# Kernel optimization log

Hardware: AMD Instinct MI355X
Metric: run time of the kernel (lower is better)

## Reference

```python
import jax, jax.numpy as jnp
import numpy as np

NUM_EMB = 1024
EMB_DIM = 256
COMM_COST = 0.25
BETA = 0.25


def setup_inputs() -> dict:
    key = jax.random.key(0)
    k1, k2 = jax.random.split(key)
    x = jax.random.normal(k1, (16, EMB_DIM, 64, 64), dtype=jnp.float32)
    # nn.Embedding initialized uniform(-1/num_emb, 1/num_emb)
    emb_weight = jax.random.uniform(
        k2, (NUM_EMB, EMB_DIM), dtype=jnp.float32,
        minval=-1.0 / NUM_EMB, maxval=1.0 / NUM_EMB)
    return {"x": x, "emb_weight": emb_weight}


def reference(x, emb_weight):
    # x: [B, C, H, W] -> [B, H, W, C]
    xp = jnp.transpose(x, (0, 2, 3, 1))
    B, H, W, C = xp.shape
    flat = xp.reshape(-1, C)  # [N, C]
    # squared euclidean distances (argmin-equivalent to torch.cdist)
    d2 = (jnp.sum(flat * flat, axis=1, keepdims=True)
          - 2.0 * jnp.einsum('nc,kc->nk', flat, emb_weight)
          + jnp.sum(emb_weight * emb_weight, axis=1))  # [N, K]
    idx = jnp.argmin(d2, axis=1)  # [N]
    quantized = emb_weight[idx].reshape(B, H, W, C)
    e_latent_loss = jnp.mean((jax.lax.stop_gradient(quantized) - xp) ** 2) * BETA
    q_latent_loss = jnp.mean((quantized - jax.lax.stop_gradient(xp)) ** 2)
    c_loss = q_latent_loss + COMM_COST * e_latent_loss
    # straight-through estimator
    quant_st = xp + jax.lax.stop_gradient(quantized - xp)
    quant_out = jnp.transpose(quant_st, (0, 3, 1, 2))  # [B, C, H, W]
    return (c_loss, quant_out)
```

## Files before the change

### kernel.cpp

```cpp
#include <hip/hip_runtime.h>
#include <hip/hip_bf16.h>
#include <cstdint>
#include <cstddef>

#define EMB_K   1024
#define EMB_C   256
#define HWB     4096
#define NPIX    65536

typedef __bf16 bf16x8 __attribute__((ext_vector_type(8)));
typedef float  f32x4  __attribute__((ext_vector_type(4)));

__device__ __forceinline__ unsigned short bf16bits(float v) {
  __hip_bfloat16 h = __float2bfloat16(v);
  return __builtin_bit_cast(unsigned short, h);
}

__global__ void k_emb(const float* __restrict__ emb, unsigned short* __restrict__ emb_bf,
                      float* __restrict__ enorm, float* __restrict__ loss) {
  int k = blockIdx.x;
  int c = threadIdx.x;
  if (k == 0 && c == 0) *loss = 0.f;
  float v = emb[(size_t)k * EMB_C + c];
  emb_bf[(size_t)k * EMB_C + c] = bf16bits(v);
  float s = v * v;
  for (int m = 32; m; m >>= 1) s += __shfl_down(s, m, 64);
  __shared__ float red[4];
  int lane = c & 63, w = c >> 6;
  if (lane == 0) red[w] = s;
  __syncthreads();
  if (c == 0) enorm[k] = red[0] + red[1] + red[2] + red[3];
}

__device__ __forceinline__ void stage64(const unsigned short* __restrict__ rows,
                                        unsigned char* buf, int t) {
#pragma unroll
  for (int j = 0; j < 4; ++j) {
    int d = j * 512 + t;
    int r = d >> 5;
    int slot = d & 31;
    int c16 = ((slot >> 3) << 3) | ((slot & 7) ^ (r & 7));
    const unsigned short* src = rows + (size_t)r * EMB_C + c16 * 8;
    __builtin_amdgcn_global_load_lds(
        (const __attribute__((address_space(1))) void*)src,
        (__attribute__((address_space(3))) void*)(buf + (unsigned)(j * 8192 + (t >> 6) * 1024)),
        16, 0, 0);
  }
}

__device__ __forceinline__ int posA(int cc, int nl) {
  return ((cc >> 3) << 3) | ((cc & 7) ^ ((nl ^ (nl >> 2)) & 7));
}

#define LDS_BYTES 137280

__global__ __launch_bounds__(512) void
k_main(const float* __restrict__ x, const unsigned short* __restrict__ embbf,
       const float* __restrict__ enorm, unsigned* __restrict__ keys_g,
       float* __restrict__ loss) {
  extern __shared__ char smem[];
  unsigned char* Abase = (unsigned char*)smem + 65536;
  float*    cjl    = (float*)(smem + 131072);
  unsigned* keys_l = (unsigned*)(smem + 135168);
  float*    xn_l   = (float*)(smem + 136192);
  float*    red    = (float*)(smem + 137216);

  int n0 = blockIdx.x * 256;
  int b  = n0 >> 12, hw0 = n0 & 4095;
  int t = threadIdx.x, w = t >> 6, lane = t & 63;
  int quad = lane >> 4, lr = lane & 15;
  int g  = w >> 1;
  int h2 = w & 1;

  stage64(embbf,               (unsigned char*)smem,         t);
  stage64(embbf + 64 * EMB_C,  (unsigned char*)smem + 32768, t);

  if (t < 256) { keys_l[t] = 0u; xn_l[t] = 0.f; }
  for (int i = t; i < 1024; i += 512) cjl[i] = 0.375f - 0.5f * enorm[i];
  __syncthreads();

  bf16x8 af[4][8];
#pragma unroll
  for (int p = 0; p < 2; ++p) {
    if (p) __syncthreads();
    {
      int hwq = t & 31;
      int cg  = t >> 5;
      const float* xp = x + (size_t)b * (EMB_C * HWB) + hw0 + p * 128 + hwq * 4;
      float xn[4] = {0.f, 0.f, 0.f, 0.f};
      unsigned pk[4][8] = {};
#pragma unroll
      for (int j = 0; j < 16; ++j) {
        f32x4 v = *(const f32x4*)(xp + (size_t)(cg * 16 + j) * HWB);
#pragma unroll
        for (int m = 0; m < 4; ++m) {
          xn[m] += v[m] * v[m];
          pk[m][j >> 1] |= (unsigned)bf16bits(v[m]) << ((j & 1) * 16);
        }
      }
#pragma unroll
      for (int m = 0; m < 4; ++m) {
        int nl = hwq * 4 + m;
        *(uint4*)(Abase + nl * 512 + posA(cg * 2,     nl) * 16) = *(const uint4*)&pk[m][0];
        *(uint4*)(Abase + nl * 512 + posA(cg * 2 + 1, nl) * 16) = *(const uint4*)&pk[m][4];
        atomicAdd(&xn_l[p * 128 + nl], xn[m]);
      }
    }
    __syncthreads();
    if ((g >> 1) == p) {
#pragma unroll
      for (int i = 0; i < 4; ++i) {
        int rA = (g & 1) * 64 + i * 16 + lr;
#pragma unroll
        for (int s = 0; s < 8; ++s) {
          int cc = s * 4 + quad;
          af[i][s] = *(const bf16x8*)(Abase + rA * 512 + posA(cc, rA) * 16);
        }
      }
    }
  }
  __syncthreads();

  unsigned best[4][4] = {};
  for (int kt = 0; kt < 16; ++kt) {
    if (kt < 14)
      stage64(embbf + (size_t)(kt + 2) * 64 * EMB_C,
              (unsigned char*)smem + (((kt + 2) & 3) << 15), t);
    if (kt < 14)       asm volatile("s_waitcnt vmcnt(8)" ::: "memory");
    else if (kt == 14) asm volatile("s_waitcnt vmcnt(4)" ::: "memory");
    else               asm volatile("s_waitcnt vmcnt(0)" ::: "memory");
    __builtin_amdgcn_s_barrier();
    __builtin_amdgcn_sched_barrier(0);
    const unsigned char* srcB = (const unsigned char*)smem + ((kt & 3) << 15);
    float cj[2]; unsigned kp[2];
#pragma unroll
    for (int j = 0; j < 2; ++j) {
      int k = kt * 64 + h2 * 32 + j * 16 + lr;
      cj[j] = cjl[k];
      kp[j] = 1023u - (unsigned)k;
    }
    f32x4 acc[4][2] = {};
#pragma unroll
    for (int s = 0; s < 8; ++s) {
      int cc = s * 4 + quad;
      int pos = ((cc >> 3) << 3) | ((cc & 7) ^ (lr & 7));
      bf16x8 bf[2];
#pragma unroll
      for (int j = 0; j < 2; ++j)
        bf[j] = *(const bf16x8*)(srcB + (h2 * 32 + j * 16 + lr) * 512 + pos * 16);
#pragma unroll
      for (int i = 0; i < 4; ++i)
#pragma unroll
        for (int j = 0; j < 2; ++j)
          acc[i][j] = __builtin_amdgcn_mfma_f32_16x16x32_bf16(af[i][s], bf[j], acc[i][j], 0, 0, 0);
    }
#pragma unroll
    for (int i = 0; i < 4; ++i)
#pragma unroll
      for (int j = 0; j < 2; ++j)
#pragma unroll
        for (int r = 0; r < 4; ++r) {
          float f = acc[i][j][r] + cj[j];
          unsigned key = (__float_as_uint(f) & 0xFFFFFC00u) | kp[j];
          best[i][r] = best[i][r] > key ? best[i][r] : key;
        }
  }
  __syncthreads();

#pragma unroll
  for (int i = 0; i < 4; ++i)
#pragma unroll
    for (int r = 0; r < 4; ++r) {
      unsigned v = best[i][r];
#pragma unroll
      for (int m = 1; m < 16; m <<= 1) {
        unsigned o = (unsigned)__shfl_xor((int)v, m, 64);
        v = v > o ? v : o;
      }
      if (lr == 0) atomicMax(&keys_l[g * 64 + i * 16 + quad * 4 + r], v);
    }
  __syncthreads();

  if (t < 256) {
    unsigned key = keys_l[t];
    keys_g[n0 + t] = key;
    float fh = __uint_as_float(key & 0xFFFFFC00u);
    float lsum = xn_l[t] + 0.75f - 2.0f * fh;
    for (int m = 32; m; m >>= 1) lsum += __shfl_down(lsum, m, 64);
    if (lane == 0) red[w] = lsum;
  }
  __syncthreads();
  if (t == 0)
    atomicAdd(loss, red[0] + red[1] + red[2] + red[3]);
}

__global__ __launch_bounds__(256) void
k_out(const float* __restrict__ emb, const unsigned* __restrict__ keys_g,
      const float* __restrict__ loss, float* __restrict__ out) {
  __shared__ float tile[64 * 65];
  __shared__ int   idx_l[64];
  int e  = blockIdx.x;
  int nt = e >> 1, cH = e & 1;
  int n0 = nt * 64;
  int b  = n0 >> 12, hw0 = n0 & 4095;
  int t = threadIdx.x, w = t >> 6, lane = t & 63;
  if (e == 0 && t == 0)
    out[0] = 1.0625f * (*loss) / 16777216.0f;
  if (t < 64) idx_l[t] = 1023 - (int)(keys_g[n0 + t] & 1023u);
  __syncthreads();
  int nn = t >> 2, ch = t & 3;
  const float* er = emb + (size_t)idx_l[nn] * EMB_C + cH * 128;
  float* ob = out + 1 + (size_t)b * (EMB_C * HWB) + (size_t)cH * 128 * HWB + hw0;
  for (int p = 0; p < 2; ++p) {
    if (p) __syncthreads();
#pragma unroll
    for (int q = 0; q < 4; ++q) {
      f32x4 v = *(const f32x4*)(er + p * 64 + q * 16 + ch * 4);
#pragma unroll
      for (int m = 0; m < 4; ++m)
        tile[(q * 16 + ch * 4 + m) * 65 + nn] = v[m];
    }
    __syncthreads();
#pragma unroll
    for (int cc = 0; cc < 16; ++cc) {
      int cl = w * 16 + cc;
      ob[(size_t)(p * 64 + cl) * HWB + lane] = tile[cl * 65 + lane];
    }
  }
}

extern "C" void kernel_launch(void* const* d_in, const int* in_sizes, int n_in,
                              void* d_out, int out_size, void* d_ws, size_t ws_size,
                              hipStream_t stream) {
  const float* x   = (const float*)d_in[0];
  const float* emb = (const float*)d_in[1];
  float* out = (float*)d_out;
  char*  ws  = (char*)d_ws;

  unsigned short* emb_bf = (unsigned short*)ws;
  float*          enorm  = (float*)(ws + 524288);
  float*          loss   = (float*)(ws + 528384);
  unsigned*       keys_g = (unsigned*)(ws + 532480);

  hipFuncSetAttribute((const void*)k_main,
                      hipFuncAttributeMaxDynamicSharedMemorySize, LDS_BYTES);

  k_emb <<<dim3(EMB_K),      dim3(EMB_C), 0,         stream>>>(emb, emb_bf, enorm, loss);
  k_main<<<dim3(NPIX / 256), dim3(512),   LDS_BYTES, stream>>>(x, emb_bf, enorm,
                                                               keys_g, loss);
  k_out <<<dim3(NPIX / 32),  dim3(256),   0,         stream>>>(emb, keys_g, loss, out);
}
```

Measured before the change: 156.9 us.

## Split x transpose/bf16 pack into separate kernel writing MFMA-fragment layout

Adds a pre-pass kernel that reads x, converts it to bf16 in the exact per-lane MFMA A-fragment order, stores it in the output buffer as scratch, and writes per-pixel squared norms to workspace. The main kernel then loads its A fragments directly from global memory with coalesced 16-byte loads, dropping the in-kernel transpose through LDS and two barriers. This spreads the strided x reads across more, smaller blocks to improve parallelism, at the cost of an extra launch and an additional write and read of the bf16 activations (about 32 MB) through global memory. The output buffer is reused as scratch before k_out overwrites it.

```diff
diff --git a/kernel.cpp b/kernel.cpp
--- a/kernel.cpp
+++ b/kernel.cpp
@@ -32,6 +32,43 @@
   if (c == 0) enorm[k] = red[0] + red[1] + red[2] + red[3];
 }
 
+__global__ __launch_bounds__(512) void
+k_tr(const float* __restrict__ x, unsigned short* __restrict__ A,
+     float* __restrict__ xn_g) {
+  __shared__ float xn_l[64];
+  int t  = threadIdx.x;
+  int n0 = blockIdx.x * 64;
+  int b  = n0 >> 12, hw0 = n0 & 4095;
+  int hwq = t & 15, c8 = t >> 4;
+  if (t < 64) xn_l[t] = 0.f;
+  __syncthreads();
+  const float* xp = x + (size_t)b * (EMB_C * HWB) + hw0 + hwq * 4;
+  float xn[4] = {0.f, 0.f, 0.f, 0.f};
+  unsigned pk[4][4] = {};
+#pragma unroll
+  for (int j = 0; j < 8; ++j) {
+    f32x4 v = *(const f32x4*)(xp + (size_t)(c8 * 8 + j) * HWB);
+#pragma unroll
+    for (int m = 0; m < 4; ++m) {
+      xn[m] += v[m] * v[m];
+      pk[m][j >> 1] |= (unsigned)bf16bits(v[m]) << ((j & 1) * 16);
+    }
+  }
+  int s = c8 >> 2, quad = c8 & 3;
+  uint4* A16 = (uint4*)A;
+#pragma unroll
+  for (int m = 0; m < 4; ++m) {
+    int n  = n0 + hwq * 4 + m;
+    int blk = n >> 8, nl = n & 255;
+    int g = nl >> 6, i = (nl >> 4) & 3, lr = nl & 15;
+    A16[(size_t)blk * 8192 + ((g * 4 + i) * 8 + s) * 64 + quad * 16 + lr]
+        = *(const uint4*)pk[m];
+    atomicAdd(&xn_l[hwq * 4 + m], xn[m]);
+  }
+  __syncthreads();
+  if (t < 64) xn_g[n0 + t] = xn_l[t];
+}
+
 __device__ __forceinline__ void stage64(const unsigned short* __restrict__ rows,
                                         unsigned char* buf, int t) {
 #pragma unroll
@@ -48,25 +85,19 @@
   }
 }
 
-__device__ __forceinline__ int posA(int cc, int nl) {
-  return ((cc >> 3) << 3) | ((cc & 7) ^ ((nl ^ (nl >> 2)) & 7));
-}
-
 #define LDS_BYTES 137280
 
 __global__ __launch_bounds__(512) void
-k_main(const float* __restrict__ x, const unsigned short* __restrict__ embbf,
-       const float* __restrict__ enorm, unsigned* __restrict__ keys_g,
-       float* __restrict__ loss) {
+k_main(const unsigned short* __restrict__ A, const unsigned short* __restrict__ embbf,
+       const float* __restrict__ enorm, const float* __restrict__ xn_g,
+       unsigned* __restrict__ keys_g, float* __restrict__ loss) {
   extern __shared__ char smem[];
-  unsigned char* Abase = (unsigned char*)smem + 65536;
   float*    cjl    = (float*)(smem + 131072);
   unsigned* keys_l = (unsigned*)(smem + 135168);
   float*    xn_l   = (float*)(smem + 136192);
   float*    red    = (float*)(smem + 137216);
 
   int n0 = blockIdx.x * 256;
-  int b  = n0 >> 12, hw0 = n0 & 4095;
   int t = threadIdx.x, w = t >> 6, lane = t & 63;
   int quad = lane >> 4, lr = lane & 15;
   int g  = w >> 1;
@@ -75,50 +106,18 @@
   stage64(embbf,               (unsigned char*)smem,         t);
   stage64(embbf + 64 * EMB_C,  (unsigned char*)smem + 32768, t);
 
-  if (t < 256) { keys_l[t] = 0u; xn_l[t] = 0.f; }
+  if (t < 256) { keys_l[t] = 0u; xn_l[t] = xn_g[n0 + t]; }
   for (int i = t; i < 1024; i += 512) cjl[i] = 0.375f - 0.5f * enorm[i];
-  __syncthreads();
 
   bf16x8 af[4][8];
-#pragma unroll
-  for (int p = 0; p < 2; ++p) {
-    if (p) __syncthreads();
-    {
-      int hwq = t & 31;
-      int cg  = t >> 5;
-      const float* xp = x + (size_t)b * (EMB_C * HWB) + hw0 + p * 128 + hwq * 4;
-      float xn[4] = {0.f, 0.f, 0.f, 0.f};
-      unsigned pk[4][8] = {};
-#pragma unroll
-      for (int j = 0; j < 16; ++j) {
-        f32x4 v = *(const f32x4*)(xp + (size_t)(cg * 16 + j) * HWB);
-#pragma unroll
-        for (int m = 0; m < 4; ++m) {
-          xn[m] += v[m] * v[m];
-          pk[m][j >> 1] |= (unsigned)bf16bits(v[m]) << ((j & 1) * 16);
-        }
-      }
-#pragma unroll
-      for (int m = 0; m < 4; ++m) {
-        int nl = hwq * 4 + m;
-        *(uint4*)(Abase + nl * 512 + posA(cg * 2,     nl) * 16) = *(const uint4*)&pk[m][0];
-        *(uint4*)(Abase + nl * 512 + posA(cg * 2 + 1, nl) * 16) = *(const uint4*)&pk[m][4];
-        atomicAdd(&xn_l[p * 128 + nl], xn[m]);
-      }
-    }
-    __syncthreads();
-    if ((g >> 1) == p) {
-#pragma unroll
-      for (int i = 0; i < 4; ++i) {
-        int rA = (g & 1) * 64 + i * 16 + lr;
-#pragma unroll
-        for (int s = 0; s < 8; ++s) {
-          int cc = s * 4 + quad;
-          af[i][s] = *(const bf16x8*)(Abase + rA * 512 + posA(cc, rA) * 16);
-        }
-      }
-    }
-  }
+  const uint4* Ab = (const uint4*)A + (size_t)blockIdx.x * 8192;
+#pragma unroll
+  for (int i = 0; i < 4; ++i)
+#pragma unroll
+    for (int s = 0; s < 8; ++s) {
+      uint4 q = Ab[((g * 4 + i) * 8 + s) * 64 + lane];
+      af[i][s] = __builtin_bit_cast(bf16x8, q);
+    }
   __syncthreads();
 
   unsigned best[4][4] = {};
@@ -240,13 +239,17 @@
   unsigned short* emb_bf = (unsigned short*)ws;
   float*          enorm  = (float*)(ws + 524288);
   float*          loss   = (float*)(ws + 528384);
-  unsigned*       keys_g = (unsigned*)(ws + 532480);
+  float*          xn_g   = (float*)(ws + 532480);
+  unsigned*       keys_g = (unsigned*)(ws + 794624);
+
+  unsigned short* A = (unsigned short*)(out + 4);
 
   hipFuncSetAttribute((const void*)k_main,
                       hipFuncAttributeMaxDynamicSharedMemorySize, LDS_BYTES);
 
   k_emb <<<dim3(EMB_K),      dim3(EMB_C), 0,         stream>>>(emb, emb_bf, enorm, loss);
-  k_main<<<dim3(NPIX / 256), dim3(512),   LDS_BYTES, stream>>>(x, emb_bf, enorm,
+  k_tr  <<<dim3(NPIX / 64),  dim3(512),   0,         stream>>>(x, A, xn_g);
+  k_main<<<dim3(NPIX / 256), dim3(512),   LDS_BYTES, stream>>>(A, emb_bf, enorm, xn_g,
                                                                keys_g, loss);
   k_out <<<dim3(NPIX / 32),  dim3(256),   0,         stream>>>(emb, keys_g, loss, out);
 }
```

Result: slower. 172.4 us (+9.9%).

## Pre-permute bf16 codebook into MFMA fragment order and replace LDS atomics for norms

Applied to the files above, without the earlier changes.

The codebook conversion kernel now writes bf16 embeddings in a tiled layout matching the MFMA B-fragment order. Staging becomes a linear copy and each lane reads its fragment with a contiguous 16-byte LDS load, with no swizzle arithmetic. The per-pixel squared-norm accumulation replaces shared-memory atomicAdd with a shuffle plus a partial-sum buffer reduced by 128 threads, at the cost of 4KB extra LDS. The layout change couples the producer kernel and the consumer indexing, so both must stay consistent.

```diff
diff --git a/kernel.cpp b/kernel.cpp
--- a/kernel.cpp
+++ b/kernel.cpp
@@ -22,27 +22,26 @@
   int c = threadIdx.x;
   if (k == 0 && c == 0) *loss = 0.f;
   float v = emb[(size_t)k * EMB_C + c];
-  emb_bf[(size_t)k * EMB_C + c] = bf16bits(v);
-  float s = v * v;
-  for (int m = 32; m; m >>= 1) s += __shfl_down(s, m, 64);
+  int kt = k >> 6, g2 = (k >> 4) & 3, lr = k & 15;
+  int s = c >> 5, quad = (c >> 3) & 3, j = c & 7;
+  size_t chunk = (size_t)kt * 2048 + (size_t)((g2 * 8 + s) * 64 + quad * 16 + lr);
+  emb_bf[chunk * 8 + j] = bf16bits(v);
+  float sq = v * v;
+  for (int m = 32; m; m >>= 1) sq += __shfl_down(sq, m, 64);
   __shared__ float red[4];
   int lane = c & 63, w = c >> 6;
-  if (lane == 0) red[w] = s;
+  if (lane == 0) red[w] = sq;
   __syncthreads();
   if (c == 0) enorm[k] = red[0] + red[1] + red[2] + red[3];
 }
 
-__device__ __forceinline__ void stage64(const unsigned short* __restrict__ rows,
+__device__ __forceinline__ void stage64(const unsigned short* __restrict__ tile_src,
                                         unsigned char* buf, int t) {
 #pragma unroll
   for (int j = 0; j < 4; ++j) {
     int d = j * 512 + t;
-    int r = d >> 5;
-    int slot = d & 31;
-    int c16 = ((slot >> 3) << 3) | ((slot & 7) ^ (r & 7));
-    const unsigned short* src = rows + (size_t)r * EMB_C + c16 * 8;
     __builtin_amdgcn_global_load_lds(
-        (const __attribute__((address_space(1))) void*)src,
+        (const __attribute__((address_space(1))) void*)(tile_src + (size_t)d * 8),
         (__attribute__((address_space(3))) void*)(buf + (unsigned)(j * 8192 + (t >> 6) * 1024)),
         16, 0, 0);
   }
@@ -52,7 +51,7 @@
   return ((cc >> 3) << 3) | ((cc & 7) ^ ((nl ^ (nl >> 2)) & 7));
 }
 
-#define LDS_BYTES 137280
+#define LDS_BYTES 141376
 
 __global__ __launch_bounds__(512) void
 k_main(const float* __restrict__ x, const unsigned short* __restrict__ embbf,
@@ -63,7 +62,8 @@
   float*    cjl    = (float*)(smem + 131072);
   unsigned* keys_l = (unsigned*)(smem + 135168);
   float*    xn_l   = (float*)(smem + 136192);
-  float*    red    = (float*)(smem + 137216);
+  float*    xn_p   = (float*)(smem + 137216);
+  float*    red    = (float*)(smem + 141312);
 
   int n0 = blockIdx.x * 256;
   int b  = n0 >> 12, hw0 = n0 & 4095;
@@ -72,10 +72,10 @@
   int g  = w >> 1;
   int h2 = w & 1;
 
-  stage64(embbf,               (unsigned char*)smem,         t);
-  stage64(embbf + 64 * EMB_C,  (unsigned char*)smem + 32768, t);
-
-  if (t < 256) { keys_l[t] = 0u; xn_l[t] = 0.f; }
+  stage64(embbf,          (unsigned char*)smem,         t);
+  stage64(embbf + 16384,  (unsigned char*)smem + 32768, t);
+
+  if (t < 256) keys_l[t] = 0u;
   for (int i = t; i < 1024; i += 512) cjl[i] = 0.375f - 0.5f * enorm[i];
   __syncthreads();
 
@@ -83,11 +83,11 @@
 #pragma unroll
   for (int p = 0; p < 2; ++p) {
     if (p) __syncthreads();
+    int hwq = t & 31;
+    int cg  = t >> 5;
+    float xn[4] = {0.f, 0.f, 0.f, 0.f};
     {
-      int hwq = t & 31;
-      int cg  = t >> 5;
       const float* xp = x + (size_t)b * (EMB_C * HWB) + hw0 + p * 128 + hwq * 4;
-      float xn[4] = {0.f, 0.f, 0.f, 0.f};
       unsigned pk[4][8] = {};
 #pragma unroll
       for (int j = 0; j < 16; ++j) {
@@ -103,10 +103,21 @@
         int nl = hwq * 4 + m;
         *(uint4*)(Abase + nl * 512 + posA(cg * 2,     nl) * 16) = *(const uint4*)&pk[m][0];
         *(uint4*)(Abase + nl * 512 + posA(cg * 2 + 1, nl) * 16) = *(const uint4*)&pk[m][4];
-        atomicAdd(&xn_l[p * 128 + nl], xn[m]);
-      }
+      }
+    }
+#pragma unroll
+    for (int m = 0; m < 4; ++m) xn[m] += __shfl_xor(xn[m], 32, 64);
+    if (lane < 32) {
+#pragma unroll
+      for (int m = 0; m < 4; ++m) xn_p[w * 128 + lane * 4 + m] = xn[m];
     }
     __syncthreads();
+    if (t < 128) {
+      float sum = 0.f;
+#pragma unroll
+      for (int ww = 0; ww < 8; ++ww) sum += xn_p[ww * 128 + t];
+      xn_l[p * 128 + t] = sum;
+    }
     if ((g >> 1) == p) {
 #pragma unroll
       for (int i = 0; i < 4; ++i) {
@@ -124,14 +135,14 @@
   unsigned best[4][4] = {};
   for (int kt = 0; kt < 16; ++kt) {
     if (kt < 14)
-      stage64(embbf + (size_t)(kt + 2) * 64 * EMB_C,
+      stage64(embbf + (size_t)(kt + 2) * 16384,
               (unsigned char*)smem + (((kt + 2) & 3) << 15), t);
     if (kt < 14)       asm volatile("s_waitcnt vmcnt(8)" ::: "memory");
     else if (kt == 14) asm volatile("s_waitcnt vmcnt(4)" ::: "memory");
     else               asm volatile("s_waitcnt vmcnt(0)" ::: "memory");
     __builtin_amdgcn_s_barrier();
     __builtin_amdgcn_sched_barrier(0);
-    const unsigned char* srcB = (const unsigned char*)smem + ((kt & 3) << 15);
+    const uint4* sb = (const uint4*)(smem + ((kt & 3) << 15));
     float cj[2]; unsigned kp[2];
 #pragma unroll
     for (int j = 0; j < 2; ++j) {
@@ -142,12 +153,12 @@
     f32x4 acc[4][2] = {};
 #pragma unroll
     for (int s = 0; s < 8; ++s) {
-      int cc = s * 4 + quad;
-      int pos = ((cc >> 3) << 3) | ((cc & 7) ^ (lr & 7));
       bf16x8 bf[2];
 #pragma unroll
-      for (int j = 0; j < 2; ++j)
-        bf[j] = *(const bf16x8*)(srcB + (h2 * 32 + j * 16 + lr) * 512 + pos * 16);
+      for (int j = 0; j < 2; ++j) {
+        uint4 q = sb[((h2 * 2 + j) * 8 + s) * 64 + lane];
+        bf[j] = __builtin_bit_cast(bf16x8, q);
+      }
 #pragma unroll
       for (int i = 0; i < 4; ++i)
 #pragma unroll
```

Result: faster. 152.9 us (-2.5%).
